# Kernel tuning notes

Hardware: AMD Instinct MI355X
Metric: run time of the kernel (lower is better)

Reference implementation:

```python
import jax, jax.numpy as jnp
import numpy as np

DIM = 1024
NUM_HEADS = 16
HEAD_DIM = DIM // NUM_HEADS


def setup_inputs() -> dict:
    key = jax.random.key(0)
    k1, k2, k3 = jax.random.split(key, 3)
    B, T = 2, 2048
    x = jax.random.normal(k1, (B, T, DIM), dtype=jnp.float32)
    w_qkv = jax.random.normal(k2, (DIM, 3 * DIM), dtype=jnp.float32) * (DIM ** -0.5)
    b_qkv = jnp.zeros((3 * DIM,), dtype=jnp.float32)
    w_proj = jax.random.normal(k3, (DIM, DIM), dtype=jnp.float32) * (DIM ** -0.5)
    b_proj = jnp.zeros((DIM,), dtype=jnp.float32)
    return {"x": x, "w_qkv": w_qkv, "b_qkv": b_qkv, "w_proj": w_proj, "b_proj": b_proj}


def reference(x, w_qkv, b_qkv, w_proj, b_proj):
    B, T, C = x.shape
    H, D = NUM_HEADS, HEAD_DIM
    scale = jnp.asarray(D ** -0.5, dtype=x.dtype)
    # qkv projection -> (B, T, 3, H, D)
    qkv = (x @ w_qkv + b_qkv).reshape(B, T, 3, H, D)
    q = qkv[:, :, 0].transpose(0, 2, 1, 3)  # (B, H, T, D)
    k = qkv[:, :, 1].transpose(0, 2, 1, 3)
    v = qkv[:, :, 2].transpose(0, 2, 1, 3)
    q = q * scale
    # scores (B, H, T, T), softmax in fp32 as in the original
    attn = jnp.einsum('bhqd,bhkd->bhqk', q, k)
    attn = jax.nn.softmax(attn.astype(jnp.float32), axis=-1).astype(v.dtype)
    out = jnp.einsum('bhqk,bhkd->bhqd', attn, v)  # (B, H, T, D)
    out = out.transpose(0, 2, 1, 3).reshape(B, T, C)
    return out @ w_proj + b_proj
```

## Files before the change

kernel.cpp:

```cpp
#include <hip/hip_runtime.h>

typedef __attribute__((ext_vector_type(8))) short short8;
typedef __attribute__((ext_vector_type(4))) float f32x4;

#define DIM_C 1024
#define NHEAD 16
#define HDIM  64
#define BB    2
#define TT    2048
#define NELEM ((size_t)BB * NHEAD * TT * HDIM)

__device__ __forceinline__ short f2b(float f) {
    union { float f; unsigned u; } c; c.f = f;
    unsigned r = c.u + 0x7FFFu + ((c.u >> 16) & 1u);
    return (short)(r >> 16);
}
__device__ __forceinline__ float b2f(short s) {
    union { unsigned u; float f; } c; c.u = ((unsigned)(unsigned short)s) << 16;
    return c.f;
}
__device__ __forceinline__ void gload_lds16(const short* g, short* l) {
    __builtin_amdgcn_global_load_lds(
        (const __attribute__((address_space(1))) unsigned int*)g,
        (__attribute__((address_space(3))) unsigned int*)l, 16, 0, 0);
}

__global__ __launch_bounds__(256) void split_f32(const float* __restrict__ X,
                                                 short* __restrict__ H,
                                                 short* __restrict__ L, int n4)
{
    const int i = blockIdx.x * 256 + threadIdx.x;
    if (i >= n4) return;
    float4 v = ((const float4*)X)[i];
    short h0 = f2b(v.x), h1 = f2b(v.y), h2 = f2b(v.z), h3 = f2b(v.w);
    short l0 = f2b(v.x - b2f(h0)), l1 = f2b(v.y - b2f(h1));
    short l2 = f2b(v.z - b2f(h2)), l3 = f2b(v.w - b2f(h3));
    typedef __attribute__((ext_vector_type(4))) short short4v;
    ((short4v*)H)[i] = (short4v){h0, h1, h2, h3};
    ((short4v*)L)[i] = (short4v){l0, l1, l2, l3};
}

__global__ __launch_bounds__(256) void transpose_split(const float* __restrict__ W,
                                                       short* __restrict__ Th,
                                                       short* __restrict__ Tl,
                                                       int K, int N)
{
    __shared__ float T[32][33];
    const int tx = threadIdx.x & 31, ty = threadIdx.x >> 5;
    const int n0 = blockIdx.x * 32, k0 = blockIdx.y * 32;
#pragma unroll
    for (int i = 0; i < 4; ++i)
        T[ty + i * 8][tx] = W[(size_t)(k0 + ty + i * 8) * N + n0 + tx];
    __syncthreads();
#pragma unroll
    for (int i = 0; i < 4; ++i) {
        const int n = ty + i * 8;
        const float v = T[tx][n];
        const short hi = f2b(v);
        Th[(size_t)(n0 + n) * K + k0 + tx] = hi;
        Tl[(size_t)(n0 + n) * K + k0 + tx] = f2b(v - b2f(hi));
    }
}

template <int EPI>
__global__ __launch_bounds__(512, 4) void gemm_mfma(
    const short* __restrict__ Ah, const short* __restrict__ Al,
    const short* __restrict__ BTh, const short* __restrict__ BTl,
    const float* __restrict__ bias,
    float* __restrict__ outF,
    short* __restrict__ qh_, short* __restrict__ ql_,
    short* __restrict__ kh_, short* __restrict__ kl_,
    short* __restrict__ vh_, short* __restrict__ vl_,
    int M, int N, int K)
{
    __shared__ short As_h[2][128 * 32];
    __shared__ short As_l[2][128 * 32];
    __shared__ short Bs_h[2][128 * 32];
    __shared__ short Bs_l[2][128 * 32];

    const int tid  = threadIdx.x;
    const int lane = tid & 63;
    const int wid  = tid >> 6;
    const int wr   = wid >> 2;
    const int wc   = wid & 3;
    const int g    = lane >> 4, lr = lane & 15;
    const int row0 = blockIdx.y * 128;
    const int col0 = blockIdx.x * 128;
    const int KT   = K >> 5;

    const int sr  = tid >> 2;
    const int ss  = (tid & 3) ^ ((sr >> 1) & 3);
    const size_t srcAb = (size_t)(row0 + sr) * K + ss * 8;
    const size_t srcBb = (size_t)(col0 + sr) * K + ss * 8;

    auto STAGE = [&](int kt, int b) {
        const size_t ka = srcAb + kt * 32;
        const size_t kb = srcBb + kt * 32;
        gload_lds16(Ah + ka, &As_h[b][tid * 8]);
        gload_lds16(Al + ka, &As_l[b][tid * 8]);
        gload_lds16(BTh + kb, &Bs_h[b][tid * 8]);
        gload_lds16(BTl + kb, &Bs_l[b][tid * 8]);
    };

    f32x4 acc[4][2];
#pragma unroll
    for (int m = 0; m < 4; ++m)
#pragma unroll
        for (int n = 0; n < 2; ++n) acc[m][n] = (f32x4){0.f, 0.f, 0.f, 0.f};

    STAGE(0, 0);
    STAGE(1, 1);

    for (int t = 0; t < KT; ++t) {
        const int c = t & 1;
        if (t == KT - 1) { asm volatile("s_waitcnt vmcnt(0)" ::: "memory"); }
        else             { asm volatile("s_waitcnt vmcnt(4)" ::: "memory"); }
        __builtin_amdgcn_sched_barrier(0);
        __builtin_amdgcn_s_barrier();
        __builtin_amdgcn_sched_barrier(0);

        short8 bhf[2], blf[2];
#pragma unroll
        for (int mh = 0; mh < 2; ++mh) {
            if (mh == 0) {
#pragma unroll
                for (int n = 0; n < 2; ++n) {
                    const int r  = wc * 32 + n * 16 + lr;
                    const int sl = g ^ ((r >> 1) & 3);
                    bhf[n] = *(const short8*)&Bs_h[c][r * 32 + sl * 8];
                    blf[n] = *(const short8*)&Bs_l[c][r * 32 + sl * 8];
                }
            }
            short8 ahf[2], alf[2];
#pragma unroll
            for (int m2 = 0; m2 < 2; ++m2) {
                const int r  = wr * 64 + (mh * 2 + m2) * 16 + lr;
                const int sl = g ^ ((r >> 1) & 3);
                ahf[m2] = *(const short8*)&As_h[c][r * 32 + sl * 8];
                alf[m2] = *(const short8*)&As_l[c][r * 32 + sl * 8];
            }
            asm volatile("s_waitcnt lgkmcnt(0)" ::: "memory");
            __builtin_amdgcn_sched_barrier(0);
            __builtin_amdgcn_s_setprio(1);
#pragma unroll
            for (int m2 = 0; m2 < 2; ++m2)
#pragma unroll
                for (int n = 0; n < 2; ++n) {
                    const int m = mh * 2 + m2;
                    acc[m][n] = __builtin_amdgcn_mfma_f32_16x16x32_bf16(ahf[m2], bhf[n], acc[m][n], 0, 0, 0);
                    acc[m][n] = __builtin_amdgcn_mfma_f32_16x16x32_bf16(alf[m2], bhf[n], acc[m][n], 0, 0, 0);
                    acc[m][n] = __builtin_amdgcn_mfma_f32_16x16x32_bf16(ahf[m2], blf[n], acc[m][n], 0, 0, 0);
                }
            __builtin_amdgcn_s_setprio(0);
            __builtin_amdgcn_sched_barrier(0);
            __builtin_amdgcn_s_barrier();
            __builtin_amdgcn_sched_barrier(0);
        }
        if (t + 2 < KT) STAGE(t + 2, c);
    }

#pragma unroll
    for (int m = 0; m < 4; ++m) {
#pragma unroll
        for (int n = 0; n < 2; ++n) {
#pragma unroll
            for (int r = 0; r < 4; ++r) {
                const int grow = row0 + wr * 64 + m * 16 + g * 4 + r;
                const int gcol = col0 + wc * 32 + n * 16 + lr;
                const float vv = acc[m][n][r] + bias[gcol];
                if (EPI == 0) {
                    const int b     = grow / TT;
                    const int t     = grow % TT;
                    const int which = gcol >> 10;
                    const int rem   = gcol & 1023;
                    const int h     = rem >> 6;
                    const int d     = rem & 63;
                    if (which == 0) {
                        const size_t idx = (((size_t)(b * NHEAD + h)) * TT + t) * HDIM + d;
                        const float sv = vv * 0.125f;
                        const short hi = f2b(sv);
                        qh_[idx] = hi; ql_[idx] = f2b(sv - b2f(hi));
                    } else if (which == 1) {
                        const size_t idx = (((size_t)(b * NHEAD + h)) * TT + t) * HDIM + d;
                        const short hi = f2b(vv);
                        kh_[idx] = hi; kl_[idx] = f2b(vv - b2f(hi));
                    } else {
                        const int t32 = t & 31;
                        const int u = t32 >> 4, gq = (t32 >> 2) & 3, rr = t32 & 3;
                        const int tp = (t & ~31) | (gq * 8 + u * 4 + rr);
                        const size_t idx = ((size_t)((b * NHEAD + h) * HDIM + d)) * TT + tp;
                        const short hi = f2b(vv);
                        vh_[idx] = hi; vl_[idx] = f2b(vv - b2f(hi));
                    }
                } else {
                    outF[(size_t)grow * N + gcol] = vv;
                }
            }
        }
    }
}

__global__ __launch_bounds__(256, 2) void attn_mfma(
    const short* __restrict__ qh, const short* __restrict__ ql,
    const short* __restrict__ kh, const short* __restrict__ kl,
    const short* __restrict__ vth, const short* __restrict__ vtl,
    short* __restrict__ oh, short* __restrict__ ol)
{
    __shared__ short Kh_s[2][4096];
    __shared__ short Kl_s[2][4096];
    __shared__ short Vh_s[2][4096];
    __shared__ short Vl_s[2][4096];

    const int tid  = threadIdx.x;
    const int wid  = tid >> 6;
    const int lane = tid & 63;
    const int g    = lane >> 4;
    const int lr   = lane & 15;
    const int lr7  = lr & 7;

    const int bid = (blockIdx.x & 7) * (gridDim.x >> 3) + (blockIdx.x >> 3);
    const int bh  = bid >> 4;
    const int q0  = (bid & 15) * 128;
    const size_t base = (size_t)bh * TT * HDIM;

    short8 qhf[2][2], qlf[2][2];
#pragma unroll
    for (int qs = 0; qs < 2; ++qs) {
        const size_t qrow = base + (size_t)(q0 + wid * 32 + qs * 16 + lr) * HDIM;
#pragma unroll
        for (int ks = 0; ks < 2; ++ks) {
            qhf[qs][ks] = *(const short8*)(qh + qrow + ks * 32 + g * 8);
            qlf[qs][ks] = *(const short8*)(ql + qrow + ks * 32 + g * 8);
        }
    }

    f32x4 ofr[2][4];
#pragma unroll
    for (int qs = 0; qs < 2; ++qs)
#pragma unroll
        for (int dt = 0; dt < 4; ++dt) ofr[qs][dt] = (f32x4){0.f, 0.f, 0.f, 0.f};
    float lsum[2] = {0.f, 0.f};

    auto STAGE = [&](int bsel, int step) {
#pragma unroll
        for (int i = 0; i < 2; ++i) {
            const int c   = tid + i * 256;
            const int row = c >> 3;
            const int sl  = (c & 7) ^ (row & 7);
            const size_t srcK = base + (size_t)(step * 64 + row) * HDIM + sl * 8;
            const size_t srcV = ((size_t)(bh * HDIM + row)) * TT + step * 64 + sl * 8;
            gload_lds16(kh + srcK, &Kh_s[bsel][c * 8]);
            gload_lds16(kl + srcK, &Kl_s[bsel][c * 8]);
            gload_lds16(vth + srcV, &Vh_s[bsel][c * 8]);
            gload_lds16(vtl + srcV, &Vl_s[bsel][c * 8]);
        }
    };

    STAGE(0, 0);
    __syncthreads();

    for (int step = 0; step < TT / 64; ++step) {
        const int cur = step & 1;
        if (step + 1 < TT / 64) STAGE(cur ^ 1, step + 1);

        f32x4 sfr[4][2];
#pragma unroll
        for (int t = 0; t < 4; ++t)
#pragma unroll
            for (int qs = 0; qs < 2; ++qs) sfr[t][qs] = (f32x4){0.f, 0.f, 0.f, 0.f};
#pragma unroll
        for (int t = 0; t < 4; ++t) {
#pragma unroll
            for (int ks = 0; ks < 2; ++ks) {
                const int adr = (t * 16 + lr) * 64 + (((ks * 4 + g) ^ lr7) * 8);
                short8 k8h = *(const short8*)&Kh_s[cur][adr];
                short8 k8l = *(const short8*)&Kl_s[cur][adr];
#pragma unroll
                for (int qs = 0; qs < 2; ++qs) {
                    sfr[t][qs] = __builtin_amdgcn_mfma_f32_16x16x32_bf16(k8h, qhf[qs][ks], sfr[t][qs], 0, 0, 0);
                    sfr[t][qs] = __builtin_amdgcn_mfma_f32_16x16x32_bf16(k8l, qhf[qs][ks], sfr[t][qs], 0, 0, 0);
                    sfr[t][qs] = __builtin_amdgcn_mfma_f32_16x16x32_bf16(k8h, qlf[qs][ks], sfr[t][qs], 0, 0, 0);
                }
            }
        }

        short8 pah[2][2], pal[2][2];
#pragma unroll
        for (int qs = 0; qs < 2; ++qs)
#pragma unroll
            for (int ks = 0; ks < 2; ++ks)
#pragma unroll
                for (int t2 = 0; t2 < 2; ++t2) {
                    const int t = ks * 2 + t2;
#pragma unroll
                    for (int r = 0; r < 4; ++r) {
                        const float p = __expf(sfr[t][qs][r]);
                        lsum[qs] += p;
                        const short hi = f2b(p);
                        pah[qs][ks][t2 * 4 + r] = hi;
                        pal[qs][ks][t2 * 4 + r] = f2b(p - b2f(hi));
                    }
                }

#pragma unroll
        for (int dt = 0; dt < 4; ++dt) {
#pragma unroll
            for (int ks = 0; ks < 2; ++ks) {
                const int adr = (dt * 16 + lr) * 64 + (((ks * 4 + g) ^ lr7) * 8);
                short8 v8h = *(const short8*)&Vh_s[cur][adr];
                short8 v8l = *(const short8*)&Vl_s[cur][adr];
#pragma unroll
                for (int qs = 0; qs < 2; ++qs) {
                    ofr[qs][dt] = __builtin_amdgcn_mfma_f32_16x16x32_bf16(pah[qs][ks], v8h, ofr[qs][dt], 0, 0, 0);
                    ofr[qs][dt] = __builtin_amdgcn_mfma_f32_16x16x32_bf16(pal[qs][ks], v8h, ofr[qs][dt], 0, 0, 0);
                    ofr[qs][dt] = __builtin_amdgcn_mfma_f32_16x16x32_bf16(pah[qs][ks], v8l, ofr[qs][dt], 0, 0, 0);
                }
            }
        }
        __syncthreads();
    }

#pragma unroll
    for (int qs = 0; qs < 2; ++qs) {
        lsum[qs] += __shfl_xor(lsum[qs], 16, 64);
        lsum[qs] += __shfl_xor(lsum[qs], 32, 64);
    }
    float rl[2][4];
#pragma unroll
    for (int qs = 0; qs < 2; ++qs)
#pragma unroll
        for (int r = 0; r < 4; ++r)
            rl[qs][r] = 1.f / __shfl(lsum[qs], g * 4 + r, 64);

    const int b = bh >> 4, h = bh & 15;
#pragma unroll
    for (int qs = 0; qs < 2; ++qs)
#pragma unroll
        for (int r = 0; r < 4; ++r) {
            const int t = q0 + wid * 32 + qs * 16 + g * 4 + r;
#pragma unroll
            for (int dt = 0; dt < 4; ++dt) {
                const float v = ofr[qs][dt][r] * rl[qs][r];
                const short hi = f2b(v);
                const size_t off = ((size_t)b * TT + t) * DIM_C + h * HDIM + dt * 16 + lr;
                oh[off] = hi;
                ol[off] = f2b(v - b2f(hi));
            }
        }
}

extern "C" void kernel_launch(void* const* d_in, const int* in_sizes, int n_in,
                              void* d_out, int out_size, void* d_ws, size_t ws_size,
                              hipStream_t stream)
{
    const float* x      = (const float*)d_in[0];
    const float* w_qkv  = (const float*)d_in[1];
    const float* b_qkv  = (const float*)d_in[2];
    const float* w_proj = (const float*)d_in[3];
    const float* b_proj = (const float*)d_in[4];
    float* out = (float*)d_out;

    char* wsb = (char*)d_ws;
    const size_t MB = 1024 * 1024;
    short* xh_w = (short*)(wsb + 0 * MB);
    short* xl_w = (short*)(wsb + 8 * MB);
    short* oh_w = xh_w;
    short* ol_w = xl_w;
    short* wqTh = (short*)(wsb + 16 * MB);
    short* wqTl = (short*)(wsb + 22 * MB);
    short* wpTh = (short*)(wsb + 16 * MB);
    short* wpTl = (short*)(wsb + 18 * MB);
    short* qh_w = (short*)(wsb + 28 * MB);
    short* ql_w = (short*)(wsb + 36 * MB);
    short* kh_w = (short*)(wsb + 44 * MB);
    short* kl_w = (short*)(wsb + 52 * MB);
    short* vth_w = (short*)(wsb + 60 * MB);
    short* vtl_w = (short*)(wsb + 68 * MB);

    split_f32<<<dim3(NELEM / 4 / 256), 256, 0, stream>>>(x, xh_w, xl_w, NELEM / 4);
    transpose_split<<<dim3(3 * DIM_C / 32, DIM_C / 32), 256, 0, stream>>>(
        w_qkv, wqTh, wqTl, DIM_C, 3 * DIM_C);

    dim3 g1(3 * DIM_C / 128, BB * TT / 128);
    gemm_mfma<0><<<g1, 512, 0, stream>>>(xh_w, xl_w, wqTh, wqTl, b_qkv, nullptr,
                                         qh_w, ql_w, kh_w, kl_w, vth_w, vtl_w,
                                         BB * TT, 3 * DIM_C, DIM_C);

    transpose_split<<<dim3(DIM_C / 32, DIM_C / 32), 256, 0, stream>>>(
        w_proj, wpTh, wpTl, DIM_C, DIM_C);

    attn_mfma<<<dim3(512), 256, 0, stream>>>(
        qh_w, ql_w, kh_w, kl_w, vth_w, vtl_w, oh_w, ol_w);

    dim3 g2(DIM_C / 128, BB * TT / 128);
    gemm_mfma<1><<<g2, 512, 0, stream>>>(oh_w, ol_w, wpTh, wpTl, b_proj, out,
                                         nullptr, nullptr, nullptr, nullptr, nullptr, nullptr,
                                         BB * TT, DIM_C, DIM_C);
}
```

Measured before the change: 355.1 us.

## Enlarge GEMM tiles to 256x256 with dynamic LDS and XCD-swizzled 1D grid

The split-bf16 GEMM moves from 128x128 to 256x256 output tiles per 512-thread block, using 128KB of dynamic shared memory. The block index is now a 1D grid remapped through an XCD-aware swizzle. The pipeline changes to prefetch the next K-slab before computing the current one, with a single barrier per step. Larger tiles raise data reuse per LDS load. In exchange, the projection GEMM now launches only 64 blocks, far fewer than the CU count, and the 128-register accumulator per thread risks register pressure or spills.

```diff
diff --git a/kernel.cpp b/kernel.cpp
--- a/kernel.cpp
+++ b/kernel.cpp
@@ -63,7 +63,7 @@
 }
 
 template <int EPI>
-__global__ __launch_bounds__(512, 4) void gemm_mfma(
+__global__ __launch_bounds__(512, 2) void gemm_mfma(
     const short* __restrict__ Ah, const short* __restrict__ Al,
     const short* __restrict__ BTh, const short* __restrict__ BTl,
     const float* __restrict__ bias,
@@ -73,10 +73,11 @@
     short* __restrict__ vh_, short* __restrict__ vl_,
     int M, int N, int K)
 {
-    __shared__ short As_h[2][128 * 32];
-    __shared__ short As_l[2][128 * 32];
-    __shared__ short Bs_h[2][128 * 32];
-    __shared__ short Bs_l[2][128 * 32];
+    extern __shared__ short smem[];
+    short* const Ah_s = smem;
+    short* const Al_s = smem + 16384;
+    short* const Bh_s = smem + 32768;
+    short* const Bl_s = smem + 49152;
 
     const int tid  = threadIdx.x;
     const int lane = tid & 63;
@@ -84,89 +85,87 @@
     const int wr   = wid >> 2;
     const int wc   = wid & 3;
     const int g    = lane >> 4, lr = lane & 15;
-    const int row0 = blockIdx.y * 128;
-    const int col0 = blockIdx.x * 128;
+
+    const int nbx = N >> 8;
+    const int nwg = gridDim.x;
+    const int swzb = (blockIdx.x & 7) * (nwg >> 3) + (blockIdx.x >> 3);
+    const int col0 = (swzb % nbx) * 256;
+    const int row0 = (swzb / nbx) * 256;
     const int KT   = K >> 5;
 
-    const int sr  = tid >> 2;
-    const int ss  = (tid & 3) ^ ((sr >> 1) & 3);
-    const size_t srcAb = (size_t)(row0 + sr) * K + ss * 8;
-    const size_t srcBb = (size_t)(col0 + sr) * K + ss * 8;
+    const int c0 = tid, c1 = tid + 512;
+    const int r0 = c0 >> 2, gs0 = (c0 & 3) ^ ((r0 >> 1) & 3);
+    const int r1 = c1 >> 2, gs1 = (c1 & 3) ^ ((r1 >> 1) & 3);
+    const size_t srcA0 = (size_t)(row0 + r0) * K + gs0 * 8;
+    const size_t srcA1 = (size_t)(row0 + r1) * K + gs1 * 8;
+    const size_t srcB0 = (size_t)(col0 + r0) * K + gs0 * 8;
+    const size_t srcB1 = (size_t)(col0 + r1) * K + gs1 * 8;
 
     auto STAGE = [&](int kt, int b) {
-        const size_t ka = srcAb + kt * 32;
-        const size_t kb = srcBb + kt * 32;
-        gload_lds16(Ah + ka, &As_h[b][tid * 8]);
-        gload_lds16(Al + ka, &As_l[b][tid * 8]);
-        gload_lds16(BTh + kb, &Bs_h[b][tid * 8]);
-        gload_lds16(BTl + kb, &Bs_l[b][tid * 8]);
+        const int d0 = b * 8192 + c0 * 8;
+        const int d1 = b * 8192 + c1 * 8;
+        const size_t ko = (size_t)kt * 32;
+        gload_lds16(Ah  + srcA0 + ko, Ah_s + d0);
+        gload_lds16(Ah  + srcA1 + ko, Ah_s + d1);
+        gload_lds16(Al  + srcA0 + ko, Al_s + d0);
+        gload_lds16(Al  + srcA1 + ko, Al_s + d1);
+        gload_lds16(BTh + srcB0 + ko, Bh_s + d0);
+        gload_lds16(BTh + srcB1 + ko, Bh_s + d1);
+        gload_lds16(BTl + srcB0 + ko, Bl_s + d0);
+        gload_lds16(BTl + srcB1 + ko, Bl_s + d1);
     };
 
-    f32x4 acc[4][2];
-#pragma unroll
-    for (int m = 0; m < 4; ++m)
-#pragma unroll
-        for (int n = 0; n < 2; ++n) acc[m][n] = (f32x4){0.f, 0.f, 0.f, 0.f};
+    f32x4 acc[8][4];
+#pragma unroll
+    for (int m = 0; m < 8; ++m)
+#pragma unroll
+        for (int n = 0; n < 4; ++n) acc[m][n] = (f32x4){0.f, 0.f, 0.f, 0.f};
 
     STAGE(0, 0);
-    STAGE(1, 1);
+    asm volatile("s_waitcnt vmcnt(0)" ::: "memory");
+    __builtin_amdgcn_sched_barrier(0);
+    __builtin_amdgcn_s_barrier();
+    __builtin_amdgcn_sched_barrier(0);
 
     for (int t = 0; t < KT; ++t) {
-        const int c = t & 1;
-        if (t == KT - 1) { asm volatile("s_waitcnt vmcnt(0)" ::: "memory"); }
-        else             { asm volatile("s_waitcnt vmcnt(4)" ::: "memory"); }
+        const int cur = t & 1;
+        if (t + 1 < KT) STAGE(t + 1, cur ^ 1);
+
+        short8 bhf[4], blf[4];
+#pragma unroll
+        for (int n = 0; n < 4; ++n) {
+            const int r = wc * 64 + n * 16 + lr;
+            const int p = g ^ ((r >> 1) & 3);
+            bhf[n] = *(const short8*)&Bh_s[cur * 8192 + r * 32 + p * 8];
+            blf[n] = *(const short8*)&Bl_s[cur * 8192 + r * 32 + p * 8];
+        }
+#pragma unroll
+        for (int m = 0; m < 8; ++m) {
+            const int r = wr * 128 + m * 16 + lr;
+            const int p = g ^ ((r >> 1) & 3);
+            short8 ah = *(const short8*)&Ah_s[cur * 8192 + r * 32 + p * 8];
+            short8 al = *(const short8*)&Al_s[cur * 8192 + r * 32 + p * 8];
+#pragma unroll
+            for (int n = 0; n < 4; ++n) {
+                acc[m][n] = __builtin_amdgcn_mfma_f32_16x16x32_bf16(ah, bhf[n], acc[m][n], 0, 0, 0);
+                acc[m][n] = __builtin_amdgcn_mfma_f32_16x16x32_bf16(al, bhf[n], acc[m][n], 0, 0, 0);
+                acc[m][n] = __builtin_amdgcn_mfma_f32_16x16x32_bf16(ah, blf[n], acc[m][n], 0, 0, 0);
+            }
+        }
+        asm volatile("s_waitcnt vmcnt(0)" ::: "memory");
         __builtin_amdgcn_sched_barrier(0);
         __builtin_amdgcn_s_barrier();
         __builtin_amdgcn_sched_barrier(0);
-
-        short8 bhf[2], blf[2];
-#pragma unroll
-        for (int mh = 0; mh < 2; ++mh) {
-            if (mh == 0) {
-#pragma unroll
-                for (int n = 0; n < 2; ++n) {
-                    const int r  = wc * 32 + n * 16 + lr;
-                    const int sl = g ^ ((r >> 1) & 3);
-                    bhf[n] = *(const short8*)&Bs_h[c][r * 32 + sl * 8];
-                    blf[n] = *(const short8*)&Bs_l[c][r * 32 + sl * 8];
-                }
-            }
-            short8 ahf[2], alf[2];
-#pragma unroll
-            for (int m2 = 0; m2 < 2; ++m2) {
-                const int r  = wr * 64 + (mh * 2 + m2) * 16 + lr;
-                const int sl = g ^ ((r >> 1) & 3);
-                ahf[m2] = *(const short8*)&As_h[c][r * 32 + sl * 8];
-                alf[m2] = *(const short8*)&As_l[c][r * 32 + sl * 8];
-            }
-            asm volatile("s_waitcnt lgkmcnt(0)" ::: "memory");
-            __builtin_amdgcn_sched_barrier(0);
-            __builtin_amdgcn_s_setprio(1);
-#pragma unroll
-            for (int m2 = 0; m2 < 2; ++m2)
-#pragma unroll
-                for (int n = 0; n < 2; ++n) {
-                    const int m = mh * 2 + m2;
-                    acc[m][n] = __builtin_amdgcn_mfma_f32_16x16x32_bf16(ahf[m2], bhf[n], acc[m][n], 0, 0, 0);
-                    acc[m][n] = __builtin_amdgcn_mfma_f32_16x16x32_bf16(alf[m2], bhf[n], acc[m][n], 0, 0, 0);
-                    acc[m][n] = __builtin_amdgcn_mfma_f32_16x16x32_bf16(ahf[m2], blf[n], acc[m][n], 0, 0, 0);
-                }
-            __builtin_amdgcn_s_setprio(0);
-            __builtin_amdgcn_sched_barrier(0);
-            __builtin_amdgcn_s_barrier();
-            __builtin_amdgcn_sched_barrier(0);
-        }
-        if (t + 2 < KT) STAGE(t + 2, c);
-    }
-
-#pragma unroll
-    for (int m = 0; m < 4; ++m) {
-#pragma unroll
-        for (int n = 0; n < 2; ++n) {
+    }
+
+#pragma unroll
+    for (int m = 0; m < 8; ++m) {
+#pragma unroll
+        for (int n = 0; n < 4; ++n) {
 #pragma unroll
             for (int r = 0; r < 4; ++r) {
-                const int grow = row0 + wr * 64 + m * 16 + g * 4 + r;
-                const int gcol = col0 + wc * 32 + n * 16 + lr;
+                const int grow = row0 + wr * 128 + m * 16 + g * 4 + r;
+                const int gcol = col0 + wc * 64 + n * 16 + lr;
                 const float vv = acc[m][n][r] + bias[gcol];
                 if (EPI == 0) {
                     const int b     = grow / TT;
@@ -377,14 +376,20 @@
     short* vth_w = (short*)(wsb + 60 * MB);
     short* vtl_w = (short*)(wsb + 68 * MB);
 
+    const int LDS_BYTES = 131072;
+    hipFuncSetAttribute((const void*)gemm_mfma<0>,
+                        hipFuncAttributeMaxDynamicSharedMemorySize, LDS_BYTES);
+    hipFuncSetAttribute((const void*)gemm_mfma<1>,
+                        hipFuncAttributeMaxDynamicSharedMemorySize, LDS_BYTES);
+
     split_f32<<<dim3(NELEM / 4 / 256), 256, 0, stream>>>(x, xh_w, xl_w, NELEM / 4);
     transpose_split<<<dim3(3 * DIM_C / 32, DIM_C / 32), 256, 0, stream>>>(
         w_qkv, wqTh, wqTl, DIM_C, 3 * DIM_C);
 
-    dim3 g1(3 * DIM_C / 128, BB * TT / 128);
-    gemm_mfma<0><<<g1, 512, 0, stream>>>(xh_w, xl_w, wqTh, wqTl, b_qkv, nullptr,
-                                         qh_w, ql_w, kh_w, kl_w, vth_w, vtl_w,
-                                         BB * TT, 3 * DIM_C, DIM_C);
+    gemm_mfma<0><<<dim3(192), 512, LDS_BYTES, stream>>>(
+        xh_w, xl_w, wqTh, wqTl, b_qkv, nullptr,
+        qh_w, ql_w, kh_w, kl_w, vth_w, vtl_w,
+        BB * TT, 3 * DIM_C, DIM_C);
 
     transpose_split<<<dim3(DIM_C / 32, DIM_C / 32), 256, 0, stream>>>(
         w_proj, wpTh, wpTl, DIM_C, DIM_C);
@@ -392,8 +397,8 @@
     attn_mfma<<<dim3(512), 256, 0, stream>>>(
         qh_w, ql_w, kh_w, kl_w, vth_w, vtl_w, oh_w, ol_w);
 
-    dim3 g2(DIM_C / 128, BB * TT / 128);
-    gemm_mfma<1><<<g2, 512, 0, stream>>>(oh_w, ol_w, wpTh, wpTl, b_proj, out,
-                                         nullptr, nullptr, nullptr, nullptr, nullptr, nullptr,
-                                         BB * TT, DIM_C, DIM_C);
-}
+    gemm_mfma<1><<<dim3(64), 512, LDS_BYTES, stream>>>(
+        oh_w, ol_w, wpTh, wpTl, b_proj, out,
+        nullptr, nullptr, nullptr, nullptr, nullptr, nullptr,
+        BB * TT, DIM_C, DIM_C);
+}
```

Result: slower. 391.8 us (+10.3%).
